# Performance work log

Measured on AMD Instinct MI355X. Metric: run time of the kernel, lower is better.

The kernel has to match this reference:

```python
import jax, jax.numpy as jnp
import numpy as np

B, V_PREV, V_NEXT = 1, 16384, 65536
F_IN, F_OUT = 512, 256
NNZ_UP, N_EDGE = 65536, 524288
EPS = 1e-5


def batch_spmm(row, col, val, m, x):
    # sparse [m, n] (COO row/col/val) @ dense x [B, n, d] -> [B, m, d]
    contrib = val[None, :, None] * x[:, col, :]          # [B, nnz, d]
    return jnp.zeros((x.shape[0], m, x.shape[2]), x.dtype).at[:, row, :].add(contrib)


def batchnorm(x, g, b):
    # BatchNorm1d in training mode: stats over (batch, node) per channel
    mu = jnp.mean(x, axis=(0, 1), keepdims=True)
    var = jnp.var(x, axis=(0, 1), keepdims=True)
    return (x - mu) * jax.lax.rsqrt(var + EPS) * g + b


def ecc(x, src, dst, w, Ui_W, Ui_b, Uj_W, Uj_b):
    # edge-conditioned graph conv: out_i = Ui(x_i) + sum_{(j->i)} w_e * Uj(x_j)
    n_nodes = x.shape[1]
    uj = x @ Uj_W + Uj_b                                  # [B, V, Fout]
    msg = w[None, :, None] * uj[:, src, :]                # [B, E, Fout]
    agg = jnp.zeros((x.shape[0], n_nodes, Uj_W.shape[1]), x.dtype).at[:, dst, :].add(msg)
    return x @ Ui_W + Ui_b + agg


def setup_inputs() -> dict:
    key = jax.random.key(0)
    ks = jax.random.split(key, 16)
    s_in = 1.0 / np.sqrt(F_IN)
    s_out = 1.0 / np.sqrt(F_OUT)
    p = {}
    p["x"] = jax.random.normal(ks[0], (B, V_PREV, F_IN), jnp.float32)
    p["up_row"] = jnp.arange(NNZ_UP, dtype=jnp.int32)
    p["up_col"] = jax.random.randint(ks[1], (NNZ_UP,), 0, V_PREV)
    p["up_val"] = jax.random.uniform(ks[2], (NNZ_UP,), jnp.float32)
    p["edge_src"] = jax.random.randint(ks[3], (N_EDGE,), 0, V_NEXT)
    p["edge_dst"] = jax.random.randint(ks[4], (N_EDGE,), 0, V_NEXT)
    p["adj_val"] = jax.random.uniform(ks[5], (N_EDGE,), jnp.float32)
    p["W_res"] = jax.random.normal(ks[6], (F_IN, F_OUT), jnp.float32) * s_in
    p["b_res"] = jnp.zeros((F_OUT,), jnp.float32)
    p["bn0_g"] = jnp.ones((F_IN,), jnp.float32)
    p["bn0_b"] = jnp.zeros((F_IN,), jnp.float32)
    p["bn1_g"] = jnp.ones((F_OUT,), jnp.float32)
    p["bn1_b"] = jnp.zeros((F_OUT,), jnp.float32)
    p["Ui0_W"] = jax.random.normal(ks[7], (F_IN, F_OUT), jnp.float32) * s_in
    p["Ui0_b"] = jnp.zeros((F_OUT,), jnp.float32)
    p["Uj0_W"] = jax.random.normal(ks[8], (F_IN, F_OUT), jnp.float32) * s_in
    p["Uj0_b"] = jnp.zeros((F_OUT,), jnp.float32)
    p["Ui1_W"] = jax.random.normal(ks[9], (F_OUT, F_OUT), jnp.float32) * s_out
    p["Ui1_b"] = jnp.zeros((F_OUT,), jnp.float32)
    p["Uj1_W"] = jax.random.normal(ks[10], (F_OUT, F_OUT), jnp.float32) * s_out
    p["Uj1_b"] = jnp.zeros((F_OUT,), jnp.float32)
    return p


def reference(x, up_row, up_col, up_val, edge_src, edge_dst, adj_val,
              W_res, b_res, bn0_g, bn0_b, bn1_g, bn1_b,
              Ui0_W, Ui0_b, Uj0_W, Uj0_b, Ui1_W, Ui1_b, Uj1_W, Uj1_b):
    # residual branch: sparse upsample then 1x1 conv (= linear over channels)
    residual = batch_spmm(up_row, up_col, up_val, V_NEXT, x)      # [B, V_NEXT, F_IN]
    residual = residual @ W_res + b_res                           # [B, V_NEXT, F_OUT]
    # main branch
    out = jax.nn.relu(batchnorm(x, bn0_g, bn0_b))                 # [B, V_PREV, F_IN]
    out = batch_spmm(up_row, up_col, up_val, V_NEXT, out)         # [B, V_NEXT, F_IN]
    out = ecc(out, edge_src, edge_dst, adj_val, Ui0_W, Ui0_b, Uj0_W, Uj0_b)
    out = jax.nn.relu(batchnorm(out, bn1_g, bn1_b))
    out = ecc(out, edge_src, edge_dst, adj_val, Ui1_W, Ui1_b, Uj1_W, Uj1_b)
    return out + residual
```

## Files before the change

### kernel.cpp

```cpp
#include <hip/hip_runtime.h>

#define V_PREV 16384
#define V_NEXT 65536
#define F_IN   512
#define F_OUT  256
#define NNZ_UP 65536
#define N_EDGE 524288

using f32x4 = __attribute__((ext_vector_type(4))) float;
using bfrag = __attribute__((ext_vector_type(8))) short;

#define LSTR 36

__device__ __forceinline__ ushort f2bf(float f) {
    union { float f; unsigned u; } v; v.f = f;
    unsigned r = (v.u + 0x7FFFu + ((v.u >> 16) & 1u)) >> 16;
    return (ushort)r;
}
__device__ __forceinline__ float bf2f(ushort h) {
    union { unsigned u; float f; } v; v.u = ((unsigned)h) << 16; return v.f;
}

__global__ void mega_prep_kernel(const float* __restrict__ Wres,
                                 const float* __restrict__ Ui0W, const float* __restrict__ Uj0W,
                                 const float* __restrict__ Ui1W, const float* __restrict__ Uj1W,
                                 const float* __restrict__ Ui1b, const float* __restrict__ bres,
                                 const int* __restrict__ up_row, const int* __restrict__ up_col,
                                 const float* __restrict__ up_val,
                                 const int* __restrict__ dst,
                                 const float* __restrict__ x,
                                 ushort* __restrict__ WresT, ushort* __restrict__ W0t,
                                 ushort* __restrict__ W1cat, float* __restrict__ biasUi,
                                 int* __restrict__ colof, float* __restrict__ valof,
                                 int* __restrict__ cnt,
                                 float* __restrict__ psum0, float* __restrict__ psq0)
{
    int b = blockIdx.x, t = threadIdx.x;
    if (b < 1024) {
        int i = b * 256 + t;
        if (i < 256 * 512) {
            int n = i / 512, k = i % 512;
            WresT[i] = f2bf(Wres[k * 256 + n]);
            W1cat[i] = f2bf(k < 256 ? Ui1W[k * 256 + n] : Uj1W[(k - 256) * 256 + n]);
        }
        {
            int n = i / 512, k = i % 512;
            W0t[i] = f2bf(n < 256 ? Uj0W[k * 256 + n] : Ui0W[k * 256 + (n - 256)]);
        }
        if (i < 256) biasUi[i] = Ui1b[i] + bres[i];
    } else if (b < 1280) {
        int k = (b - 1024) * 256 + t;
        int r = up_row[k];
        colof[r] = up_col[k];
        valof[r] = up_val[k];
    } else if (b < 3328) {
        int e = (b - 1280) * 256 + t;
        atomicAdd(&cnt[dst[e]], 1);
    } else {
        int blk = b - 3328;
        float s0 = 0, s1 = 0, q0 = 0, q1 = 0;
        for (int r = 0; r < 32; r++) {
            size_t base = ((size_t)blk * 32 + r) * 512;
            float a = x[base + t], bb = x[base + t + 256];
            s0 += a; q0 += a * a; s1 += bb; q1 += bb * bb;
        }
        psum0[blk * 512 + t] = s0; psum0[blk * 512 + t + 256] = s1;
        psq0 [blk * 512 + t] = q0; psq0 [blk * 512 + t + 256] = q1;
    }
}

__global__ void scan_block_kernel(const int* __restrict__ cnt, int* __restrict__ offs,
                                  int* __restrict__ bsum)
{
    __shared__ int buf[2][256];
    int t = threadIdx.x;
    int i = blockIdx.x * 256 + t;
    int v = cnt[i];
    int p = 0;
    buf[0][t] = v;
    __syncthreads();
    for (int d = 1; d < 256; d <<= 1) {
        int nv = buf[p][t] + ((t >= d) ? buf[p][t - d] : 0);
        buf[p ^ 1][t] = nv;
        p ^= 1;
        __syncthreads();
    }
    int incl = buf[p][t];
    offs[i] = incl - v;
    if (t == 255) bsum[blockIdx.x] = incl;
}

__global__ void add_offs_bnfin_kernel(int* __restrict__ offs, const int* __restrict__ bsum,
                                      int* __restrict__ cursor,
                                      const float* __restrict__ psum0, const float* __restrict__ psq0,
                                      const float* __restrict__ g0, const float* __restrict__ b0,
                                      float* __restrict__ sc0, float* __restrict__ sh0)
{
    int b = blockIdx.x, t = threadIdx.x;
    if (b < 256) {
        __shared__ int buf[2][256];
        int v = bsum[t];
        int p = 0;
        buf[0][t] = v;
        __syncthreads();
        for (int d = 1; d < 256; d <<= 1) {
            int nv = buf[p][t] + ((t >= d) ? buf[p][t - d] : 0);
            buf[p ^ 1][t] = nv;
            p ^= 1;
            __syncthreads();
        }
        int excl = buf[p][b] - bsum[b];
        int i = b * 256 + t;
        int o = offs[i] + excl;
        offs[i] = o;
        cursor[i] = o;
    } else {
        int vb = b - 256;
        int gw = (vb * 256 + t) >> 6;
        int lane = t & 63;
        float s = 0, q = 0;
        for (int i = lane; i < 512; i += 64) {
            s += psum0[(size_t)i * 512 + gw];
            q += psq0 [(size_t)i * 512 + gw];
        }
#pragma unroll
        for (int d = 32; d > 0; d >>= 1) {
            s += __shfl_xor(s, d);
            q += __shfl_xor(q, d);
        }
        if (lane == 0) {
            float m = s * (1.0f / V_PREV);
            float v = q * (1.0f / V_PREV) - m * m;
            float r = rsqrtf(v + 1e-5f);
            float scale = r * g0[gw];
            sc0[gw] = scale;
            sh0[gw] = b0[gw] - m * scale;
        }
    }
}

__global__ void bn_finish_kernel(const float* __restrict__ psum, const float* __restrict__ psq,
                                 int nblocks, int C, float invN,
                                 const float* __restrict__ g, const float* __restrict__ b,
                                 float* __restrict__ sc, float* __restrict__ sh)
{
    int gw = (blockIdx.x * blockDim.x + threadIdx.x) >> 6;
    int lane = threadIdx.x & 63;
    if (gw >= C) return;
    float s = 0, q = 0;
    for (int i = lane; i < nblocks; i += 64) {
        s += psum[(size_t)i * C + gw];
        q += psq [(size_t)i * C + gw];
    }
#pragma unroll
    for (int d = 32; d > 0; d >>= 1) {
        s += __shfl_xor(s, d);
        q += __shfl_xor(q, d);
    }
    if (lane == 0) {
        float m = s * invN;
        float v = q * invN - m * m;
        float r = rsqrtf(v + 1e-5f);
        float scale = r * g[gw];
        sc[gw] = scale;
        sh[gw] = b[gw] - m * scale;
    }
}

__global__ __launch_bounds__(256)
void fill_gemm0_kernel(const int* __restrict__ src, const int* __restrict__ dst,
                       const float* __restrict__ adjv,
                       const int* __restrict__ colof, const float* __restrict__ valof,
                       int* __restrict__ cursor, int4* __restrict__ E,
                       const float* __restrict__ x,
                       const ushort* __restrict__ WresT, const ushort* __restrict__ W0t,
                       const float* __restrict__ sc0, const float* __restrict__ sh0,
                       ushort* __restrict__ XW, ushort* __restrict__ XNJ,
                       ushort* __restrict__ XNI)
{
    __shared__ ushort As[128 * LSTR];
    __shared__ ushort Bs[128 * LSTR];
    __shared__ float s_sc[512], s_sh[512];

    const int tid = threadIdx.x;
    if (blockIdx.x < 2048) {
        int e = blockIdx.x * 256 + tid;
        int d = dst[e];
        int s = src[e];
        float a = adjv[e];
        int p = atomicAdd(&cursor[d], 1);
        int4 v;
        v.x = s;
        v.y = __float_as_int(a);
        v.z = colof[s];
        v.w = __float_as_int(a * valof[s]);
        E[p] = v;
        return;
    }

    const int id   = blockIdx.x - 2048;
    const int xcd  = id & 7;
    const int rest = id >> 3;
    const int slot = rest / 6;
    const int bx   = rest - slot * 6;
    const int by   = slot * 8 + xcd;

    const bool bnmode = bx >= 2;
    const ushort* Bt = bnmode ? W0t : WresT;
    const int btrow = bnmode ? (bx - 2) * 128 : bx * 128;
    ushort* Cout = (bx < 2) ? XW : (bx < 4 ? XNJ : XNI);
    const int colbase = (bx & 1) * 128;
    const int tM = by * 128;

    for (int i = tid; i < 512; i += 256) { s_sc[i] = sc0[i]; s_sh[i] = sh0[i]; }
    __syncthreads();

    const int lane = tid & 63;
    const int wave = tid >> 6;
    const int wm = wave >> 1, wn = wave & 1;
    const int lr = lane & 15, lg = lane >> 4;

    const int ra = tid >> 1;
    const int ua = (tid & 1) * 2;
    const int rb = tid >> 2;
    const int ub = tid & 3;

    f32x4 acc[4][4] = {};

    for (int k0 = 0; k0 < 512; k0 += 32) {
        const float* xp = &x[(size_t)(tM + ra) * 512 + k0 + ua * 8];
        float4 f0 = *(const float4*)(xp);
        float4 f1 = *(const float4*)(xp + 4);
        float4 f2 = *(const float4*)(xp + 8);
        float4 f3 = *(const float4*)(xp + 12);
        float vv[16] = { f0.x,f0.y,f0.z,f0.w, f1.x,f1.y,f1.z,f1.w,
                         f2.x,f2.y,f2.z,f2.w, f3.x,f3.y,f3.z,f3.w };
        ushort hh[16];
        if (bnmode) {
#pragma unroll
            for (int j = 0; j < 16; j++) {
                int c = k0 + ua * 8 + j;
                hh[j] = f2bf(fmaxf(vv[j] * s_sc[c] + s_sh[c], 0.0f));
            }
        } else {
#pragma unroll
            for (int j = 0; j < 16; j++) hh[j] = f2bf(vv[j]);
        }
        *(uint4*)&As[ra * LSTR + ua * 8]       = *(uint4*)&hh[0];
        *(uint4*)&As[ra * LSTR + (ua + 1) * 8] = *(uint4*)&hh[8];

#pragma unroll
        for (int i = 0; i < 2; i++) {
            int row = rb + i * 64;
            *(uint4*)&Bs[row * LSTR + ub * 8] =
                *(const uint4*)&Bt[(size_t)(btrow + row) * 512 + k0 + ub * 8];
        }
        __syncthreads();

        bfrag af[4], bfv[4];
#pragma unroll
        for (int mm = 0; mm < 4; mm++) {
            int row = wm * 64 + mm * 16 + lr;
            af[mm] = *(const bfrag*)&As[row * LSTR + lg * 8];
        }
#pragma unroll
        for (int nn = 0; nn < 4; nn++) {
            int row = wn * 64 + nn * 16 + lr;
            bfv[nn] = *(const bfrag*)&Bs[row * LSTR + lg * 8];
        }
#pragma unroll
        for (int mm = 0; mm < 4; mm++)
#pragma unroll
            for (int nn = 0; nn < 4; nn++)
                acc[mm][nn] = __builtin_amdgcn_mfma_f32_16x16x32_bf16(af[mm], bfv[nn], acc[mm][nn], 0, 0, 0);
        __syncthreads();
    }

#pragma unroll
    for (int mm = 0; mm < 4; mm++)
#pragma unroll
        for (int nn = 0; nn < 4; nn++)
#pragma unroll
            for (int r = 0; r < 4; r++) {
                int row = tM + wm * 64 + mm * 16 + lg * 4 + r;
                int col = colbase + wn * 64 + nn * 16 + lr;
                Cout[(size_t)row * 256 + col] = f2bf(acc[mm][nn][r]);
            }
}

__global__ __launch_bounds__(256)
void gather0_kernel(const int* __restrict__ offs, const int* __restrict__ cnt,
                    const int4* __restrict__ E,
                    const int* __restrict__ colof, const float* __restrict__ valof,
                    const ushort* __restrict__ XNJ, const ushort* __restrict__ XNI,
                    const float* __restrict__ ui_b, const float* __restrict__ uj_b,
                    ushort* __restrict__ X1, float* __restrict__ sumA,
                    float* __restrict__ psum1s, float* __restrict__ psq1s)
{
    __shared__ float redS[4][256];
    __shared__ float redQ[4][256];

    int wave = threadIdx.x >> 6;
    int lane = threadIdx.x & 63;
    int f = lane * 4;
    float ub0 = ui_b[f + 0], ub1 = ui_b[f + 1], ub2 = ui_b[f + 2], ub3 = ui_b[f + 3];
    float jb0 = uj_b[f + 0], jb1 = uj_b[f + 1], jb2 = uj_b[f + 2], jb3 = uj_b[f + 3];
    float ss0 = 0, ss1 = 0, ss2 = 0, ss3 = 0;
    float qq0 = 0, qq1 = 0, qq2 = 0, qq3 = 0;

    for (int it = 0; it < 8; it++) {
        int d = (blockIdx.x * 8 + it) * 4 + wave;
        int c = colof[d];
        float s = valof[d];
        ushort4 u = *(const ushort4*)&XNI[(size_t)c * 256 + f];
        const ushort* up = (const ushort*)&u;
        float a0 = ub0 + s * bf2f(up[0]);
        float a1 = ub1 + s * bf2f(up[1]);
        float a2 = ub2 + s * bf2f(up[2]);
        float a3 = ub3 + s * bf2f(up[3]);
        float sA = 0;

        int st = offs[d], n = cnt[d];
        for (int e0 = 0; e0 < n; e0 += 4) {
            int4 ev0 = E[st + e0];
            int4 ev1 = (e0 + 1 < n) ? E[st + e0 + 1] : make_int4(0, 0, 0, 0);
            int4 ev2 = (e0 + 2 < n) ? E[st + e0 + 2] : make_int4(0, 0, 0, 0);
            int4 ev3 = (e0 + 3 < n) ? E[st + e0 + 3] : make_int4(0, 0, 0, 0);
            float w0 = __int_as_float(ev0.w), w1 = __int_as_float(ev1.w);
            float w2 = __int_as_float(ev2.w), w3 = __int_as_float(ev3.w);
            sA += __int_as_float(ev0.y) + __int_as_float(ev1.y)
                + __int_as_float(ev2.y) + __int_as_float(ev3.y);
            ushort4 v0 = *(const ushort4*)&XNJ[(size_t)ev0.z * 256 + f];
            ushort4 v1 = *(const ushort4*)&XNJ[(size_t)ev1.z * 256 + f];
            ushort4 v2 = *(const ushort4*)&XNJ[(size_t)ev2.z * 256 + f];
            ushort4 v3 = *(const ushort4*)&XNJ[(size_t)ev3.z * 256 + f];
            const ushort* p0 = (const ushort*)&v0;
            const ushort* p1 = (const ushort*)&v1;
            const ushort* p2 = (const ushort*)&v2;
            const ushort* p3 = (const ushort*)&v3;
            a0 += w0 * bf2f(p0[0]) + w1 * bf2f(p1[0]) + w2 * bf2f(p2[0]) + w3 * bf2f(p3[0]);
            a1 += w0 * bf2f(p0[1]) + w1 * bf2f(p1[1]) + w2 * bf2f(p2[1]) + w3 * bf2f(p3[1]);
            a2 += w0 * bf2f(p0[2]) + w1 * bf2f(p1[2]) + w2 * bf2f(p2[2]) + w3 * bf2f(p3[2]);
            a3 += w0 * bf2f(p0[3]) + w1 * bf2f(p1[3]) + w2 * bf2f(p2[3]) + w3 * bf2f(p3[3]);
        }
        a0 += sA * jb0; a1 += sA * jb1; a2 += sA * jb2; a3 += sA * jb3;
        *(ushort4*)&X1[(size_t)d * 256 + f] =
            make_ushort4(f2bf(a0), f2bf(a1), f2bf(a2), f2bf(a3));
        if (lane == 0) sumA[d] = sA;
        ss0 += a0; ss1 += a1; ss2 += a2; ss3 += a3;
        qq0 += a0 * a0; qq1 += a1 * a1; qq2 += a2 * a2; qq3 += a3 * a3;
    }

    redS[wave][f + 0] = ss0; redS[wave][f + 1] = ss1;
    redS[wave][f + 2] = ss2; redS[wave][f + 3] = ss3;
    redQ[wave][f + 0] = qq0; redQ[wave][f + 1] = qq1;
    redQ[wave][f + 2] = qq2; redQ[wave][f + 3] = qq3;
    __syncthreads();
    int t = threadIdx.x;
    float ssum = redS[0][t] + redS[1][t] + redS[2][t] + redS[3][t];
    float sq   = redQ[0][t] + redQ[1][t] + redQ[2][t] + redQ[3][t];
    int slab = (blockIdx.x & 63) * 256 + t;
    atomicAdd(&psum1s[slab], ssum);
    atomicAdd(&psq1s[slab], sq);
}

__global__ __launch_bounds__(256)
void gather1G_kernel(const int* __restrict__ offs, const int* __restrict__ cnt,
                     const int4* __restrict__ E,
                     const ushort* __restrict__ X1,
                     const float* __restrict__ sc1, const float* __restrict__ sh1,
                     ushort* __restrict__ G)
{
    int d = blockIdx.x * 4 + (threadIdx.x >> 6);
    int f = (threadIdx.x & 63) * 4;
    float4 sc = *(const float4*)&sc1[f];
    float4 sh = *(const float4*)&sh1[f];
    float a0 = 0, a1 = 0, a2 = 0, a3 = 0;

    int st = offs[d], n = cnt[d];
    for (int e0 = 0; e0 < n; e0 += 4) {
        int4 ev0 = E[st + e0];
        int4 ev1 = (e0 + 1 < n) ? E[st + e0 + 1] : make_int4(0, 0, 0, 0);
        int4 ev2 = (e0 + 2 < n) ? E[st + e0 + 2] : make_int4(0, 0, 0, 0);
        int4 ev3 = (e0 + 3 < n) ? E[st + e0 + 3] : make_int4(0, 0, 0, 0);
        float w0 = __int_as_float(ev0.y), w1 = __int_as_float(ev1.y);
        float w2 = __int_as_float(ev2.y), w3 = __int_as_float(ev3.y);
        ushort4 v0 = *(const ushort4*)&X1[(size_t)ev0.x * 256 + f];
        ushort4 v1 = *(const ushort4*)&X1[(size_t)ev1.x * 256 + f];
        ushort4 v2 = *(const ushort4*)&X1[(size_t)ev2.x * 256 + f];
        ushort4 v3 = *(const ushort4*)&X1[(size_t)ev3.x * 256 + f];
        const ushort* p0 = (const ushort*)&v0;
        const ushort* p1 = (const ushort*)&v1;
        const ushort* p2 = (const ushort*)&v2;
        const ushort* p3 = (const ushort*)&v3;
        a0 += w0 * fmaxf(bf2f(p0[0]) * sc.x + sh.x, 0.0f)
            + w1 * fmaxf(bf2f(p1[0]) * sc.x + sh.x, 0.0f)
            + w2 * fmaxf(bf2f(p2[0]) * sc.x + sh.x, 0.0f)
            + w3 * fmaxf(bf2f(p3[0]) * sc.x + sh.x, 0.0f);
        a1 += w0 * fmaxf(bf2f(p0[1]) * sc.y + sh.y, 0.0f)
            + w1 * fmaxf(bf2f(p1[1]) * sc.y + sh.y, 0.0f)
            + w2 * fmaxf(bf2f(p2[1]) * sc.y + sh.y, 0.0f)
            + w3 * fmaxf(bf2f(p3[1]) * sc.y + sh.y, 0.0f);
        a2 += w0 * fmaxf(bf2f(p0[2]) * sc.z + sh.z, 0.0f)
            + w1 * fmaxf(bf2f(p1[2]) * sc.z + sh.z, 0.0f)
            + w2 * fmaxf(bf2f(p2[2]) * sc.z + sh.z, 0.0f)
            + w3 * fmaxf(bf2f(p3[2]) * sc.z + sh.z, 0.0f);
        a3 += w0 * fmaxf(bf2f(p0[3]) * sc.w + sh.w, 0.0f)
            + w1 * fmaxf(bf2f(p1[3]) * sc.w + sh.w, 0.0f)
            + w2 * fmaxf(bf2f(p2[3]) * sc.w + sh.w, 0.0f)
            + w3 * fmaxf(bf2f(p3[3]) * sc.w + sh.w, 0.0f);
    }
    *(ushort4*)&G[(size_t)d * 256 + f] =
        make_ushort4(f2bf(a0), f2bf(a1), f2bf(a2), f2bf(a3));
}

__global__ __launch_bounds__(512, 1)
void gemm_final_kernel(const ushort* __restrict__ X1, const ushort* __restrict__ G,
                       const ushort* __restrict__ W1cat,
                       const float* __restrict__ sc1, const float* __restrict__ sh1,
                       const float* __restrict__ biasUi, const float* __restrict__ uj1_b,
                       const float* __restrict__ sumA,
                       const int* __restrict__ colof, const float* __restrict__ valof,
                       const ushort* __restrict__ XW,
                       float* __restrict__ out)
{
    __shared__ ushort As[256 * LSTR];
    __shared__ ushort Bs[256 * LSTR];
    __shared__ float s_sc[256], s_sh[256];

    const int tid = threadIdx.x;
    const int tM = blockIdx.x * 256;

    if (tid < 256) { s_sc[tid] = sc1[tid]; s_sh[tid] = sh1[tid]; }
    __syncthreads();

    const int lane = tid & 63;
    const int wave = tid >> 6;
    const int wm = wave >> 1, wn = wave & 1;
    const int lr = lane & 15, lg = lane >> 4;

    f32x4 acc[4][8] = {};

    for (int k0 = 0; k0 < 512; k0 += 32) {
#pragma unroll
        for (int i = 0; i < 2; i++) {
            int idx = tid + i * 512;
            int row = idx >> 2, u = idx & 3;
            ushort h[8];
            if (k0 < 256) {
                *(uint4*)h = *(const uint4*)&X1[(size_t)(tM + row) * 256 + k0 + u * 8];
#pragma unroll
                for (int j = 0; j < 8; j++) {
                    int c = k0 + u * 8 + j;
                    h[j] = f2bf(fmaxf(bf2f(h[j]) * s_sc[c] + s_sh[c], 0.0f));
                }
            } else {
                *(uint4*)h = *(const uint4*)&G[(size_t)(tM + row) * 256 + (k0 - 256) + u * 8];
            }
            *(uint4*)&As[row * LSTR + u * 8] = *(uint4*)h;
        }
#pragma unroll
        for (int i = 0; i < 2; i++) {
            int idx = tid + i * 512;
            int row = idx >> 2, u = idx & 3;
            *(uint4*)&Bs[row * LSTR + u * 8] =
                *(const uint4*)&W1cat[(size_t)row * 512 + k0 + u * 8];
        }
        __syncthreads();

        bfrag af[4], bfv[8];
#pragma unroll
        for (int mm = 0; mm < 4; mm++) {
            int row = wm * 64 + mm * 16 + lr;
            af[mm] = *(const bfrag*)&As[row * LSTR + lg * 8];
        }
#pragma unroll
        for (int nn = 0; nn < 8; nn++) {
            int row = wn * 128 + nn * 16 + lr;
            bfv[nn] = *(const bfrag*)&Bs[row * LSTR + lg * 8];
        }
#pragma unroll
        for (int mm = 0; mm < 4; mm++)
#pragma unroll
            for (int nn = 0; nn < 8; nn++)
                acc[mm][nn] = __builtin_amdgcn_mfma_f32_16x16x32_bf16(af[mm], bfv[nn], acc[mm][nn], 0, 0, 0);
        __syncthreads();
    }

    float bUi[8], bUj[8];
#pragma unroll
    for (int nn = 0; nn < 8; nn++) {
        int col = wn * 128 + nn * 16 + lr;
        bUi[nn] = biasUi[col];
        bUj[nn] = uj1_b[col];
    }
#pragma unroll
    for (int mm = 0; mm < 4; mm++) {
#pragma unroll
        for (int r = 0; r < 4; r++) {
            int row = tM + wm * 64 + mm * 16 + lg * 4 + r;
            int c = colof[row];
            float s = valof[row];
            float sA = sumA[row];
#pragma unroll
            for (int nn = 0; nn < 8; nn++) {
                int col = wn * 128 + nn * 16 + lr;
                float v = acc[mm][nn][r] + bUi[nn] + sA * bUj[nn]
                        + s * bf2f(XW[(size_t)c * 256 + col]);
                out[(size_t)row * 256 + col] = v;
            }
        }
    }
}

extern "C" void kernel_launch(void* const* d_in, const int* in_sizes, int n_in,
                              void* d_out, int out_size, void* d_ws, size_t ws_size,
                              hipStream_t stream)
{
    const float* x      = (const float*)d_in[0];
    const int*   up_row = (const int*)  d_in[1];
    const int*   up_col = (const int*)  d_in[2];
    const float* up_val = (const float*)d_in[3];
    const int*   e_src  = (const int*)  d_in[4];
    const int*   e_dst  = (const int*)  d_in[5];
    const float* adjv   = (const float*)d_in[6];
    const float* W_res  = (const float*)d_in[7];
    const float* b_res  = (const float*)d_in[8];
    const float* bn0_g  = (const float*)d_in[9];
    const float* bn0_b  = (const float*)d_in[10];
    const float* bn1_g  = (const float*)d_in[11];
    const float* bn1_b  = (const float*)d_in[12];
    const float* Ui0_W  = (const float*)d_in[13];
    const float* Ui0_b  = (const float*)d_in[14];
    const float* Uj0_W  = (const float*)d_in[15];
    const float* Uj0_b  = (const float*)d_in[16];
    const float* Ui1_W  = (const float*)d_in[17];
    const float* Ui1_b  = (const float*)d_in[18];
    const float* Uj1_W  = (const float*)d_in[19];
    const float* Uj1_b  = (const float*)d_in[20];

    float* out = (float*)d_out;

    char* ws = (char*)d_ws;
    size_t off = 0;
    auto alloc = [&](size_t bytes) -> char* {
        char* p = ws + off;
        off = (off + bytes + 255) & ~(size_t)255;
        return p;
    };
    ushort* XW    = (ushort*)alloc((size_t)V_PREV * F_OUT * 2);
    ushort* XNJ   = (ushort*)alloc((size_t)V_PREV * F_OUT * 2);
    ushort* XNI   = (ushort*)alloc((size_t)V_PREV * F_OUT * 2);
    ushort* X1    = (ushort*)alloc((size_t)V_NEXT * F_OUT * 2);
    ushort* G     = (ushort*)alloc((size_t)V_NEXT * F_OUT * 2);
    int*    cnt   = (int*)   alloc(V_NEXT * 4);
    float*  psum1s= (float*) alloc(64 * 256 * 4);
    float*  psq1s = (float*) alloc(64 * 256 * 4);
    float*  sumA  = (float*) alloc(V_NEXT * 4);
    int*    offs  = (int*)   alloc(V_NEXT * 4);
    int*    cursor= (int*)   alloc(V_NEXT * 4);
    int*    bsum  = (int*)   alloc(256 * 4);
    int4*   E     = (int4*)  alloc((size_t)N_EDGE * 16);
    int*    colof = (int*)   alloc(V_NEXT * 4);
    float*  valof = (float*) alloc(V_NEXT * 4);
    ushort* WresT = (ushort*)alloc(256 * 512 * 2);
    ushort* W0t   = (ushort*)alloc(512 * 512 * 2);
    ushort* W1cat = (ushort*)alloc(256 * 512 * 2);
    float*  biasUi= (float*) alloc(256 * 4);
    float*  psum0 = (float*) alloc(512 * 512 * 4);
    float*  psq0  = (float*) alloc(512 * 512 * 4);
    float*  sc0   = (float*) alloc(512 * 4);
    float*  sh0   = (float*) alloc(512 * 4);
    float*  sc1   = (float*) alloc(256 * 4);
    float*  sh1   = (float*) alloc(256 * 4);
    (void)ws_size; (void)in_sizes; (void)n_in; (void)out_size;

    hipMemsetAsync(cnt, 0, (size_t)98304 * 4, stream);

    mega_prep_kernel<<<3840, 256, 0, stream>>>(W_res, Ui0_W, Uj0_W, Ui1_W, Uj1_W,
                                               Ui1_b, b_res,
                                               up_row, up_col, up_val,
                                               e_dst, x,
                                               WresT, W0t, W1cat, biasUi,
                                               colof, valof, cnt, psum0, psq0);

    scan_block_kernel<<<256, 256, 0, stream>>>(cnt, offs, bsum);

    add_offs_bnfin_kernel<<<384, 256, 0, stream>>>(offs, bsum, cursor,
                                                   psum0, psq0, bn0_g, bn0_b, sc0, sh0);

    fill_gemm0_kernel<<<2816, 256, 0, stream>>>(e_src, e_dst, adjv, colof, valof,
                                                cursor, E,
                                                x, WresT, W0t, sc0, sh0,
                                                XW, XNJ, XNI);

    gather0_kernel<<<2048, 256, 0, stream>>>(offs, cnt, E, colof, valof,
                                             XNJ, XNI, Ui0_b, Uj0_b,
                                             X1, sumA, psum1s, psq1s);

    bn_finish_kernel<<<64, 256, 0, stream>>>(psum1s, psq1s, 64, 256, 1.0f / V_NEXT,
                                             bn1_g, bn1_b, sc1, sh1);

    gather1G_kernel<<<V_NEXT / 4, 256, 0, stream>>>(offs, cnt, E, X1, sc1, sh1, G);

    gemm_final_kernel<<<256, 512, 0, stream>>>(X1, G, W1cat, sc1, sh1,
                                               biasUi, Uj1_b, sumA,
                                               colof, valof, XW, out);
}
```

Baseline: 239.4 us.

## Enlarge fused GEMM0 tiles to 256x256 and batch edge fill per thread

```diff
diff --git a/kernel.cpp b/kernel.cpp
--- a/kernel.cpp
+++ b/kernel.cpp
@@ -167,7 +167,7 @@
     }
 }
 
-__global__ __launch_bounds__(256)
+__global__ __launch_bounds__(512, 1)
 void fill_gemm0_kernel(const int* __restrict__ src, const int* __restrict__ dst,
                        const float* __restrict__ adjv,
                        const int* __restrict__ colof, const float* __restrict__ valof,
@@ -178,41 +178,44 @@
                        ushort* __restrict__ XW, ushort* __restrict__ XNJ,
                        ushort* __restrict__ XNI)
 {
-    __shared__ ushort As[128 * LSTR];
-    __shared__ ushort Bs[128 * LSTR];
+    __shared__ ushort As[256 * LSTR];
+    __shared__ ushort Bs[256 * LSTR];
     __shared__ float s_sc[512], s_sh[512];
 
     const int tid = threadIdx.x;
-    if (blockIdx.x < 2048) {
-        int e = blockIdx.x * 256 + tid;
-        int d = dst[e];
-        int s = src[e];
-        float a = adjv[e];
-        int p = atomicAdd(&cursor[d], 1);
-        int4 v;
-        v.x = s;
-        v.y = __float_as_int(a);
-        v.z = colof[s];
-        v.w = __float_as_int(a * valof[s]);
-        E[p] = v;
+    if (blockIdx.x >= 192) {
+        int base = (blockIdx.x - 192) * 4096;
+#pragma unroll
+        for (int i = 0; i < 8; i++) {
+            int e = base + i * 512 + tid;
+            int d = dst[e];
+            int s = src[e];
+            float a = adjv[e];
+            int p = atomicAdd(&cursor[d], 1);
+            int4 v;
+            v.x = s;
+            v.y = __float_as_int(a);
+            v.z = colof[s];
+            v.w = __float_as_int(a * valof[s]);
+            E[p] = v;
+        }
         return;
     }
 
-    const int id   = blockIdx.x - 2048;
+    const int id   = blockIdx.x;
     const int xcd  = id & 7;
     const int rest = id >> 3;
-    const int slot = rest / 6;
-    const int bx   = rest - slot * 6;
+    const int slot = rest / 3;
+    const int bx   = rest - slot * 3;
     const int by   = slot * 8 + xcd;
-
-    const bool bnmode = bx >= 2;
+    const int tM   = by * 256;
+
+    const bool bnmode = bx >= 1;
     const ushort* Bt = bnmode ? W0t : WresT;
-    const int btrow = bnmode ? (bx - 2) * 128 : bx * 128;
-    ushort* Cout = (bx < 2) ? XW : (bx < 4 ? XNJ : XNI);
-    const int colbase = (bx & 1) * 128;
-    const int tM = by * 128;
-
-    for (int i = tid; i < 512; i += 256) { s_sc[i] = sc0[i]; s_sh[i] = sh0[i]; }
+    const int btrow = bnmode ? (bx - 1) * 256 : 0;
+    ushort* Cout = (bx == 0) ? XW : (bx == 1 ? XNJ : XNI);
+
+    s_sc[tid] = sc0[tid]; s_sh[tid] = sh0[tid];
     __syncthreads();
 
     const int lane = tid & 63;
@@ -220,58 +223,54 @@
     const int wm = wave >> 1, wn = wave & 1;
     const int lr = lane & 15, lg = lane >> 4;
 
-    const int ra = tid >> 1;
-    const int ua = (tid & 1) * 2;
-    const int rb = tid >> 2;
-    const int ub = tid & 3;
-
-    f32x4 acc[4][4] = {};
+    f32x4 acc[4][8] = {};
 
     for (int k0 = 0; k0 < 512; k0 += 32) {
-        const float* xp = &x[(size_t)(tM + ra) * 512 + k0 + ua * 8];
-        float4 f0 = *(const float4*)(xp);
-        float4 f1 = *(const float4*)(xp + 4);
-        float4 f2 = *(const float4*)(xp + 8);
-        float4 f3 = *(const float4*)(xp + 12);
-        float vv[16] = { f0.x,f0.y,f0.z,f0.w, f1.x,f1.y,f1.z,f1.w,
-                         f2.x,f2.y,f2.z,f2.w, f3.x,f3.y,f3.z,f3.w };
-        ushort hh[16];
-        if (bnmode) {
-#pragma unroll
-            for (int j = 0; j < 16; j++) {
-                int c = k0 + ua * 8 + j;
-                hh[j] = f2bf(fmaxf(vv[j] * s_sc[c] + s_sh[c], 0.0f));
+#pragma unroll
+        for (int i = 0; i < 2; i++) {
+            int idx = tid + i * 512;
+            int row = idx >> 2, u = idx & 3;
+            const float* xp = &x[(size_t)(tM + row) * 512 + k0 + u * 8];
+            float4 f0 = *(const float4*)(xp);
+            float4 f1 = *(const float4*)(xp + 4);
+            float vv[8] = { f0.x, f0.y, f0.z, f0.w, f1.x, f1.y, f1.z, f1.w };
+            ushort h[8];
+            if (bnmode) {
+#pragma unroll
+                for (int j = 0; j < 8; j++) {
+                    int c = k0 + u * 8 + j;
+                    h[j] = f2bf(fmaxf(vv[j] * s_sc[c] + s_sh[c], 0.0f));
+                }
+            } else {
+#pragma unroll
+                for (int j = 0; j < 8; j++) h[j] = f2bf(vv[j]);
             }
-        } else {
-#pragma unroll
-            for (int j = 0; j < 16; j++) hh[j] = f2bf(vv[j]);
-        }
-        *(uint4*)&As[ra * LSTR + ua * 8]       = *(uint4*)&hh[0];
-        *(uint4*)&As[ra * LSTR + (ua + 1) * 8] = *(uint4*)&hh[8];
-
+            *(uint4*)&As[row * LSTR + u * 8] = *(uint4*)h;
+        }
 #pragma unroll
         for (int i = 0; i < 2; i++) {
-            int row = rb + i * 64;
-            *(uint4*)&Bs[row * LSTR + ub * 8] =
-                *(const uint4*)&Bt[(size_t)(btrow + row) * 512 + k0 + ub * 8];
+            int idx = tid + i * 512;
+            int row = idx >> 2, u = idx & 3;
+            *(uint4*)&Bs[row * LSTR + u * 8] =
+                *(const uint4*)&Bt[(size_t)(btrow + row) * 512 + k0 + u * 8];
         }
         __syncthreads();
 
-        bfrag af[4], bfv[4];
+        bfrag af[4], bfv[8];
 #pragma unroll
         for (int mm = 0; mm < 4; mm++) {
             int row = wm * 64 + mm * 16 + lr;
             af[mm] = *(const bfrag*)&As[row * LSTR + lg * 8];
         }
 #pragma unroll
-        for (int nn = 0; nn < 4; nn++) {
-            int row = wn * 64 + nn * 16 + lr;
+        for (int nn = 0; nn < 8; nn++) {
+            int row = wn * 128 + nn * 16 + lr;
             bfv[nn] = *(const bfrag*)&Bs[row * LSTR + lg * 8];
         }
 #pragma unroll
         for (int mm = 0; mm < 4; mm++)
 #pragma unroll
-            for (int nn = 0; nn < 4; nn++)
+            for (int nn = 0; nn < 8; nn++)
                 acc[mm][nn] = __builtin_amdgcn_mfma_f32_16x16x32_bf16(af[mm], bfv[nn], acc[mm][nn], 0, 0, 0);
         __syncthreads();
     }
@@ -279,11 +278,11 @@
 #pragma unroll
     for (int mm = 0; mm < 4; mm++)
 #pragma unroll
-        for (int nn = 0; nn < 4; nn++)
+        for (int nn = 0; nn < 8; nn++)
 #pragma unroll
             for (int r = 0; r < 4; r++) {
                 int row = tM + wm * 64 + mm * 16 + lg * 4 + r;
-                int col = colbase + wn * 64 + nn * 16 + lr;
+                int col = wn * 128 + nn * 16 + lr;
                 Cout[(size_t)row * 256 + col] = f2bf(acc[mm][nn][r]);
             }
 }
@@ -589,10 +588,10 @@
     add_offs_bnfin_kernel<<<384, 256, 0, stream>>>(offs, bsum, cursor,
                                                    psum0, psq0, bn0_g, bn0_b, sc0, sh0);
 
-    fill_gemm0_kernel<<<2816, 256, 0, stream>>>(e_src, e_dst, adjv, colof, valof,
-                                                cursor, E,
-                                                x, WresT, W0t, sc0, sh0,
-                                                XW, XNJ, XNI);
+    fill_gemm0_kernel<<<320, 512, 0, stream>>>(e_src, e_dst, adjv, colof, valof,
+                                               cursor, E,
+                                               x, WresT, W0t, sc0, sh0,
+                                               XW, XNJ, XNI);
 
     gather0_kernel<<<2048, 256, 0, stream>>>(offs, cnt, E, colof, valof,
                                              XNJ, XNI, Ui0_b, Uj0_b,
```

After: 240.5 us. No clear change (+0.5%).
